# Kernel optimization log

Hardware: AMD Instinct MI355X
Metric: run time of the kernel (lower is better)

The kernel has to match this reference:

```python
import jax, jax.numpy as jnp
import numpy as np

BETA = 0.5
K = 4
THRESH = 1.0

@jax.custom_vjp
def atan_spike(x):
    # Heaviside forward; atan surrogate gradient (snntorch atan, alpha=2)
    return (x > 0).astype(x.dtype)

def _atan_fwd(x):
    return atan_spike(x), x

def _atan_bwd(x, g):
    return (g / (1.0 + (jnp.pi * x) ** 2),)

atan_spike.defvjp(_atan_fwd, _atan_bwd)

def leaky_scan(inputs):
    # snntorch Leaky, init_hidden=True, reset_mechanism='subtract':
    # reset_t = detach(heaviside(mem_{t-1} - thr)); mem_t = beta*mem_{t-1} + x_t - reset_t*thr; spk_t = fire(mem_t - thr)
    def step(mem, inp):
        reset = jax.lax.stop_gradient((mem - THRESH > 0).astype(inp.dtype))
        mem = BETA * mem + inp - reset * THRESH
        spk = atan_spike(mem - THRESH)
        return mem, spk
    mem0 = jnp.zeros_like(inputs[0])
    _, spks = jax.lax.scan(step, mem0, inputs)
    return spks  # (T,B,C,H,W)

def setup_inputs() -> dict:
    key = jax.random.key(0)
    k1, k2, k3, k4 = jax.random.split(key, 4)
    T, B, C, H, W = 16, 32, 256, 16, 16
    # spikes are binary events
    spk_rec = (jax.random.uniform(k1, (T, B, C, H, W)) < 0.2).astype(jnp.float32)
    mem_rec = jax.random.normal(k2, (T, B, C, H, W), dtype=jnp.float32)
    weight = jax.random.normal(k3, (C, C), dtype=jnp.float32) / np.sqrt(C)  # 1x1 conv, no bias: [out_c, in_c]
    rand_idx = jax.random.permutation(k4, B).astype(jnp.int32)  # torch.randperm(B)
    return {"spk_rec": spk_rec, "mem_rec": mem_rec, "weight": weight, "rand_idx": rand_idx}

def reference(spk_rec, mem_rec, weight, rand_idx):
    # calc_context: leaky_enc=True, spike_context=True -> spike output of Leaky over spk_rec
    context = leaky_scan(spk_rec)                      # (T,B,C,H,W)
    # apply_weight: vmap 1x1 conv == channel mixing einsum
    x_pos = jnp.einsum('tbchw,oc->tbohw', spk_rec, weight)
    x_neg = x_pos[:, rand_idx]                          # permute batch
    score_pos = jnp.exp(jnp.mean(context[:-K] * x_pos[K:], axis=(2, 3, 4))) + 1e-4  # (T-K,B)
    score_neg = jnp.exp(jnp.mean(context[:-K] * x_neg[K:], axis=(2, 3, 4))) + 1e-4  # (T-K,B)
    log_score_pos = jnp.log(score_pos)                  # (T-K,B)
    log_score_neg = jnp.log(jnp.sum(score_neg, axis=1, keepdims=True))  # (T-K,1)
    loss = jnp.mean(-log_score_pos + log_score_neg)     # scalar
    return spk_rec, loss, log_score_pos, log_score_neg
```

## Files before the change

kernel.cpp:

```cpp
#include <hip/hip_runtime.h>
#include <hip/hip_bf16.h>

#define T_   16
#define B_   32
#define C_   256
#define HW_  256
#define TP_  12
#define NE_  (B_*C_*HW_)
#define NOUT0 (T_*NE_)

typedef __attribute__((ext_vector_type(8))) short short8;
typedef __attribute__((ext_vector_type(4))) float f32x4;

#define WS_WB   0
#define WS_CTX  131072
#define WS_ACC  3276800

__global__ void k_setup(const float* __restrict__ W,
                        unsigned short* __restrict__ Wb,
                        float* __restrict__ acc) {
    int i = blockIdx.x*256 + threadIdx.x;
    __hip_bfloat16 h = __float2bfloat16(W[i]);
    Wb[i] = *(unsigned short*)&h;
    if (i < 768) acc[i] = 0.f;
}

__global__ void k_scan(const float* __restrict__ spk,
                       float* __restrict__ out,
                       unsigned* __restrict__ ctxw) {
    int e = blockIdx.x*256 + threadIdx.x;
    int lane  = threadIdx.x & 63;
    int ebase = e & ~63;
    int b   = ebase >> 16;
    int c   = (ebase >> 8) & 255;
    int hw0 = ebase & 255;
    float mem = 0.f;
    for (int t = 0; t < T_; ++t) {
        float inp = spk[t*NE_ + e];
        out[t*NE_ + e] = inp;
        float reset = (mem - 1.0f > 0.0f) ? 1.0f : 0.0f;
        mem = 0.5f*mem + inp - reset;
        if (t < TP_) {
            unsigned long long m = __ballot(mem - 1.0f > 0.0f);
            if (lane == 0) {
                int wb = ((t*B_ + b)*C_ + c)*8 + (hw0 >> 5);
                ctxw[wb]   = (unsigned)m;
                ctxw[wb+1] = (unsigned)(m >> 32);
            }
        }
    }
}

__global__ __launch_bounds__(256)
void k_gemm(const unsigned short* __restrict__ Wb,
            const float* __restrict__ spkf,
            const unsigned* __restrict__ ctxw,
            const int* __restrict__ ridx,
            float* __restrict__ spos, float* __restrict__ sneg) {
    int blk  = blockIdx.x;
    int pair = blk >> 2;
    int jblk = blk & 3;
    int t  = 4 + (pair >> 5);
    int b  = pair & 31;
    int tp = t - 4;
    int hwbase = jblk * 64;

    int wv   = threadIdx.x >> 6;
    int lane = threadIdx.x & 63;
    int quad = lane >> 4;
    int n    = lane & 15;

    __shared__ __align__(16) unsigned short Ssl[64*40];
    __shared__ unsigned ctxp[512], ctxn[512];
    __shared__ float red[8];

    f32x4 acc[4][4] = {};
    const float2* Sf = (const float2*)spkf;
    long tb_base = ((long)(t*B_ + b))*C_*HW_;

    for (int kc = 0; kc < 256; kc += 32) {
        __syncthreads();
        #pragma unroll
        for (int p = 0; p < 4; ++p) {
            int v  = threadIdx.x + p*256;
            int cl = v >> 5;
            int dw = v & 31;
            float2 d = Sf[(tb_base + (long)(kc + cl)*HW_ + hwbase)/2 + dw];
            Ssl[(2*dw    )*40 + cl] = (d.x != 0.f) ? (unsigned short)0x3F80 : 0;
            Ssl[(2*dw + 1)*40 + cl] = (d.y != 0.f) ? (unsigned short)0x3F80 : 0;
        }
        __syncthreads();
        short8 bfr[4], afr[4];
        #pragma unroll
        for (int jt = 0; jt < 4; ++jt)
            bfr[jt] = *(const short8*)&Ssl[(jt*16 + n)*40 + quad*8];
        #pragma unroll
        for (int ot = 0; ot < 4; ++ot) {
            int o = wv*64 + ot*16 + n;
            afr[ot] = *(const short8*)&Wb[o*256 + kc + quad*8];
        }
        #pragma unroll
        for (int ot = 0; ot < 4; ++ot)
            #pragma unroll
            for (int jt = 0; jt < 4; ++jt)
                acc[ot][jt] = __builtin_amdgcn_mfma_f32_16x16x32_bf16(
                                  afr[ot], bfr[jt], acc[ot][jt], 0, 0, 0);
    }

    int bneg = 0;
    for (int i = 0; i < 32; ++i) if (ridx[i] == b) bneg = i;

    __syncthreads();
    for (int i = threadIdx.x; i < 512; i += 256) {
        int o = i >> 1, w = i & 1;
        int hwword = (hwbase >> 5) + w;
        ctxp[i] = ctxw[((tp*B_ + b   )*C_ + o)*8 + hwword];
        ctxn[i] = ctxw[((tp*B_ + bneg)*C_ + o)*8 + hwword];
    }
    __syncthreads();

    float P = 0.f, Nn = 0.f;
    #pragma unroll
    for (int ot = 0; ot < 4; ++ot)
        #pragma unroll
        for (int jt = 0; jt < 4; ++jt) {
            int hwl = jt*16 + n;
            int w = hwl >> 5, bit = hwl & 31;
            #pragma unroll
            for (int r = 0; r < 4; ++r) {
                int o = wv*64 + ot*16 + quad*4 + r;
                float x = acc[ot][jt][r];
                if ((ctxp[o*2 + w] >> bit) & 1) P  += x;
                if ((ctxn[o*2 + w] >> bit) & 1) Nn += x;
            }
        }
    for (int off = 32; off; off >>= 1) {
        P  += __shfl_down(P,  off);
        Nn += __shfl_down(Nn, off);
    }
    if (lane == 0) { red[wv] = P; red[4 + wv] = Nn; }
    __syncthreads();
    if (threadIdx.x == 0)
        atomicAdd(&spos[tp*32 + b],    red[0]+red[1]+red[2]+red[3]);
    if (threadIdx.x == 1)
        atomicAdd(&sneg[tp*32 + bneg], red[4]+red[5]+red[6]+red[7]);
}

__global__ void k_final(const float* __restrict__ spos,
                        const float* __restrict__ sneg,
                        float* __restrict__ out) {
    __shared__ float lsp_s[384], sn_s[384], lsn_s[12];
    int tid = threadIdx.x;
    if (tid < 384) {
        float mp = spos[tid] * (1.f/65536.f);
        lsp_s[tid] = logf(expf(mp) + 1e-4f);
        float mn = sneg[tid] * (1.f/65536.f);
        sn_s[tid] = expf(mn) + 1e-4f;
    }
    __syncthreads();
    if (tid < 12) {
        float s = 0.f;
        for (int b = 0; b < 32; ++b) s += sn_s[tid*32 + b];
        float lsn = logf(s);
        lsn_s[tid] = lsn;
        out[NOUT0 + 1 + 384 + tid] = lsn;
    }
    __syncthreads();
    if (tid < 384) out[NOUT0 + 1 + tid] = lsp_s[tid];
    if (tid == 0) {
        float L = 0.f;
        for (int t = 0; t < 12; ++t)
            for (int b = 0; b < 32; ++b)
                L += lsn_s[t] - lsp_s[t*32 + b];
        out[NOUT0] = L * (1.f/384.f);
    }
}

extern "C" void kernel_launch(void* const* d_in, const int* in_sizes, int n_in,
                              void* d_out, int out_size, void* d_ws, size_t ws_size,
                              hipStream_t stream) {
    const float* spk  = (const float*)d_in[0];
    const float* W    = (const float*)d_in[2];
    const int*   ridx = (const int*)d_in[3];
    float* out = (float*)d_out;

    char* ws = (char*)d_ws;
    unsigned short* Wb   = (unsigned short*)(ws + WS_WB);
    unsigned*       ctxw = (unsigned*)(ws + WS_CTX);
    float*          acc  = (float*)(ws + WS_ACC);
    float*          spos = acc;
    float*          sneg = acc + 384;

    k_setup<<<256, 256, 0, stream>>>(W, Wb, acc);
    k_scan <<<NE_/256, 256, 0, stream>>>(spk, out, ctxw);
    k_gemm <<<1536, 256, 0, stream>>>(Wb, spk, ctxw, ridx, spos, sneg);
    k_final<<<1, 384, 0, stream>>>(spos, sneg, out);
}
```

Before: 341.2 us.

## Bit-pack spike inputs in scan kernel so GEMM reads compact bitmasks

The scan kernel now processes four elements per lane and also emits ballot-packed bitmasks of the input spikes for timesteps 4 and later. The GEMM kernel reads these bitmasks instead of re-reading the fp32 spike tensor, expands them once into a full 256-channel bf16 LDS tile, and then runs the K loop without per-chunk syncs. The goal is to cut GEMM global traffic by about 32x, at the cost of a larger LDS footprint, extra workspace, and a launch-bounds hint that limits registers.

```diff
diff --git a/kernel.cpp b/kernel.cpp
--- a/kernel.cpp
+++ b/kernel.cpp
@@ -14,7 +14,8 @@
 
 #define WS_WB   0
 #define WS_CTX  131072
-#define WS_ACC  3276800
+#define WS_SPK  3276800
+#define WS_ACC  7471104
 
 __global__ void k_setup(const float* __restrict__ W,
                         unsigned short* __restrict__ Wb,
@@ -27,33 +28,56 @@
 
 __global__ void k_scan(const float* __restrict__ spk,
                        float* __restrict__ out,
-                       unsigned* __restrict__ ctxw) {
-    int e = blockIdx.x*256 + threadIdx.x;
-    int lane  = threadIdx.x & 63;
-    int ebase = e & ~63;
-    int b   = ebase >> 16;
-    int c   = (ebase >> 8) & 255;
-    int hw0 = ebase & 255;
-    float mem = 0.f;
+                       unsigned* __restrict__ ctxw,
+                       unsigned* __restrict__ spkw) {
+    int wave = (blockIdx.x*256 + threadIdx.x) >> 6;
+    int lane = threadIdx.x & 63;
+    long base = (long)wave*256 + lane;
+    float m0=0.f, m1=0.f, m2=0.f, m3=0.f;
+    #pragma unroll
     for (int t = 0; t < T_; ++t) {
-        float inp = spk[t*NE_ + e];
-        out[t*NE_ + e] = inp;
-        float reset = (mem - 1.0f > 0.0f) ? 1.0f : 0.0f;
-        mem = 0.5f*mem + inp - reset;
+        long o = (long)t*NE_ + base;
+        float i0 = spk[o];
+        float i1 = spk[o+64];
+        float i2 = spk[o+128];
+        float i3 = spk[o+192];
+        out[o]     = i0;
+        out[o+64]  = i1;
+        out[o+128] = i2;
+        out[o+192] = i3;
+        if (t >= 4) {
+            unsigned long long s0 = __ballot(i0 != 0.f);
+            unsigned long long s1 = __ballot(i1 != 0.f);
+            unsigned long long s2 = __ballot(i2 != 0.f);
+            unsigned long long s3 = __ballot(i3 != 0.f);
+            if (lane < 8) {
+                unsigned long long m = (lane<2)?s0 : (lane<4)?s1 : (lane<6)?s2 : s3;
+                unsigned w = (lane & 1) ? (unsigned)(m>>32) : (unsigned)m;
+                spkw[((long)t*8192 + wave)*8 + lane] = w;
+            }
+        }
+        float r0 = (m0-1.f>0.f)?1.f:0.f; m0 = 0.5f*m0 + i0 - r0;
+        float r1 = (m1-1.f>0.f)?1.f:0.f; m1 = 0.5f*m1 + i1 - r1;
+        float r2 = (m2-1.f>0.f)?1.f:0.f; m2 = 0.5f*m2 + i2 - r2;
+        float r3 = (m3-1.f>0.f)?1.f:0.f; m3 = 0.5f*m3 + i3 - r3;
         if (t < TP_) {
-            unsigned long long m = __ballot(mem - 1.0f > 0.0f);
-            if (lane == 0) {
-                int wb = ((t*B_ + b)*C_ + c)*8 + (hw0 >> 5);
-                ctxw[wb]   = (unsigned)m;
-                ctxw[wb+1] = (unsigned)(m >> 32);
+            unsigned long long c0 = __ballot(m0-1.f>0.f);
+            unsigned long long c1 = __ballot(m1-1.f>0.f);
+            unsigned long long c2 = __ballot(m2-1.f>0.f);
+            unsigned long long c3 = __ballot(m3-1.f>0.f);
+            if (lane >= 8 && lane < 16) {
+                int j = lane - 8;
+                unsigned long long m = (j<2)?c0 : (j<4)?c1 : (j<6)?c2 : c3;
+                unsigned w = (j & 1) ? (unsigned)(m>>32) : (unsigned)m;
+                ctxw[((long)t*8192 + wave)*8 + j] = w;
             }
         }
     }
 }
 
-__global__ __launch_bounds__(256)
+__global__ __launch_bounds__(256, 2)
 void k_gemm(const unsigned short* __restrict__ Wb,
-            const float* __restrict__ spkf,
+            const unsigned* __restrict__ spkw,
             const unsigned* __restrict__ ctxw,
             const int* __restrict__ ridx,
             float* __restrict__ spos, float* __restrict__ sneg) {
@@ -70,30 +94,52 @@
     int quad = lane >> 4;
     int n    = lane & 15;
 
-    __shared__ __align__(16) unsigned short Ssl[64*40];
+    __shared__ __align__(16) unsigned short Ssl[64*264];
+    __shared__ __align__(16) unsigned Sw2[512];
     __shared__ unsigned ctxp[512], ctxn[512];
     __shared__ float red[8];
 
+    {
+        int c = threadIdx.x;
+        const uint2 w = *(const uint2*)&spkw[((long)t*8192 + b*256 + c)*8 + (hwbase>>5)];
+        Sw2[c]       = w.x;
+        Sw2[256 + c] = w.y;
+    }
+    int bneg = 0;
+    #pragma unroll
+    for (int i = 0; i < 32; ++i) if (ridx[i] == b) bneg = i;
+    for (int i = threadIdx.x; i < 512; i += 256) {
+        int o = i >> 1, w = i & 1;
+        int hwword = (hwbase >> 5) + w;
+        ctxp[i] = ctxw[((tp*B_ + b   )*C_ + o)*8 + hwword];
+        ctxn[i] = ctxw[((tp*B_ + bneg)*C_ + o)*8 + hwword];
+    }
+    __syncthreads();
+
+    #pragma unroll
+    for (int p = 0; p < 8; ++p) {
+        int v  = threadIdx.x + p*256;
+        int hw = v >> 5;
+        int c0 = (v & 31)*8;
+        int wi = hw >> 5, bit = hw & 31;
+        uint4 wa = *(const uint4*)&Sw2[wi*256 + c0];
+        uint4 wb2 = *(const uint4*)&Sw2[wi*256 + c0 + 4];
+        unsigned ww[8] = {wa.x, wa.y, wa.z, wa.w, wb2.x, wb2.y, wb2.z, wb2.w};
+        short8 s;
+        #pragma unroll
+        for (int j = 0; j < 8; ++j)
+            s[j] = (short)(((ww[j] >> bit) & 1u) ? 0x3F80 : 0);
+        *(short8*)&Ssl[hw*264 + c0] = s;
+    }
+    __syncthreads();
+
     f32x4 acc[4][4] = {};
-    const float2* Sf = (const float2*)spkf;
-    long tb_base = ((long)(t*B_ + b))*C_*HW_;
-
+    #pragma unroll
     for (int kc = 0; kc < 256; kc += 32) {
-        __syncthreads();
-        #pragma unroll
-        for (int p = 0; p < 4; ++p) {
-            int v  = threadIdx.x + p*256;
-            int cl = v >> 5;
-            int dw = v & 31;
-            float2 d = Sf[(tb_base + (long)(kc + cl)*HW_ + hwbase)/2 + dw];
-            Ssl[(2*dw    )*40 + cl] = (d.x != 0.f) ? (unsigned short)0x3F80 : 0;
-            Ssl[(2*dw + 1)*40 + cl] = (d.y != 0.f) ? (unsigned short)0x3F80 : 0;
-        }
-        __syncthreads();
         short8 bfr[4], afr[4];
         #pragma unroll
         for (int jt = 0; jt < 4; ++jt)
-            bfr[jt] = *(const short8*)&Ssl[(jt*16 + n)*40 + quad*8];
+            bfr[jt] = *(const short8*)&Ssl[(jt*16 + n)*264 + kc + quad*8];
         #pragma unroll
         for (int ot = 0; ot < 4; ++ot) {
             int o = wv*64 + ot*16 + n;
@@ -106,18 +152,6 @@
                 acc[ot][jt] = __builtin_amdgcn_mfma_f32_16x16x32_bf16(
                                   afr[ot], bfr[jt], acc[ot][jt], 0, 0, 0);
     }
-
-    int bneg = 0;
-    for (int i = 0; i < 32; ++i) if (ridx[i] == b) bneg = i;
-
-    __syncthreads();
-    for (int i = threadIdx.x; i < 512; i += 256) {
-        int o = i >> 1, w = i & 1;
-        int hwword = (hwbase >> 5) + w;
-        ctxp[i] = ctxw[((tp*B_ + b   )*C_ + o)*8 + hwword];
-        ctxn[i] = ctxw[((tp*B_ + bneg)*C_ + o)*8 + hwword];
-    }
-    __syncthreads();
 
     float P = 0.f, Nn = 0.f;
     #pragma unroll
@@ -187,12 +221,13 @@
     char* ws = (char*)d_ws;
     unsigned short* Wb   = (unsigned short*)(ws + WS_WB);
     unsigned*       ctxw = (unsigned*)(ws + WS_CTX);
+    unsigned*       spkw = (unsigned*)(ws + WS_SPK);
     float*          acc  = (float*)(ws + WS_ACC);
     float*          spos = acc;
     float*          sneg = acc + 384;
 
     k_setup<<<256, 256, 0, stream>>>(W, Wb, acc);
-    k_scan <<<NE_/256, 256, 0, stream>>>(spk, out, ctxw);
-    k_gemm <<<1536, 256, 0, stream>>>(Wb, spk, ctxw, ridx, spos, sneg);
+    k_scan <<<2048, 256, 0, stream>>>(spk, out, ctxw, spkw);
+    k_gemm <<<1536, 256, 0, stream>>>(Wb, spkw, ctxw, ridx, spos, sneg);
     k_final<<<1, 384, 0, stream>>>(spos, sneg, out);
 }
```

Measured after the change: 331.1 us. 2.9% less time.
